# Kernel optimization log

Hardware: AMD Instinct MI355X
Metric: run time of the kernel (lower is better)

The kernel has to match this reference:

```python
import jax, jax.numpy as jnp
import numpy as np

B, C, H, W = 2, 24, 256, 256
R = 7  # window_size


def setup_inputs() -> dict:
    key = jax.random.key(0)
    k1, k2 = jax.random.split(key)
    latent = jax.random.normal(k1, (B, C, H, W), dtype=jnp.float32)
    # per-pixel, per-channel dynamic filter weights, one per window position (r*r)
    weights = jax.random.uniform(k2, (B, C, R * R, H, W), dtype=jnp.float32)
    return {"latent": latent, "weights": weights, "window_size": R}


def reference(latent, weights, window_size):
    """Faithful jax version of BaseTextureDiffusion._diffusion_step.

    torch: replicate-pad -> F.unfold (kernel r) -> view(B,C,r*r,H,W)
           -> permute -> elementwise * weights -> sum over r*r.
    F.unfold enumerates kernel offsets row-major (i*r + j), matching k below.
    Instead of materializing the r*r-times-larger windows tensor, accumulate
    the weighted shifted slices directly (same math, fused traffic).
    """
    r = window_size
    pad = r // 2
    h, w = latent.shape[2], latent.shape[3]
    padded = jnp.pad(latent, ((0, 0), (0, 0), (pad, pad), (pad, pad)), mode="edge")
    out = jnp.zeros_like(latent)
    for k in range(r * r):  # fixed small loop over kernel offsets
        i, j = divmod(k, r)
        out = out + weights[:, :, k] * padded[:, :, i:i + h, j:j + w]
    return out
```

## Files before the change

kernel.cpp:

```cpp
#include <hip/hip_runtime.h>


typedef float fx4 __attribute__((ext_vector_type(4)));

constexpr int Hh = 256, Ww = 256, Rr = 7, PAD = 3;
constexpr int TILE_H = 4;
constexpr int LW  = Ww + 2 * PAD;
constexpr int LWP = 264;
constexpr int LH  = TILE_H + 2 * PAD;
constexpr int TILES_Y = Hh / TILE_H;
constexpr int PLANES  = 48;

__global__ __launch_bounds__(256) void diffusion_kernel(
    const float* __restrict__ latent,
    const float* __restrict__ weights,
    float* __restrict__ out)
{
    __shared__ __align__(16) float lds[LH * LWP];

    const int bid   = blockIdx.x;
    const int plane = bid / TILES_Y;
    const int ty0   = (bid % TILES_Y) * TILE_H;

    const float* lat  = latent  + (size_t)plane * Hh * Ww;
    const float* wgt  = weights + (size_t)plane * (Rr * Rr) * Hh * Ww;
    float*       optr = out     + (size_t)plane * Hh * Ww;

    for (int idx = threadIdx.x; idx < LH * LW; idx += 256) {
        const int ly = idx / LW;
        const int lx = idx - ly * LW;
        const int gy = min(max(ty0 + ly - PAD, 0), Hh - 1);
        const int gx = min(max(lx - PAD, 0), Ww - 1);
        lds[ly * LWP + lx] = lat[gy * Ww + gx];
    }
    __syncthreads();

    const int tx = threadIdx.x & 63;
    const int ty = threadIdx.x >> 6;
    const int x  = 4 * tx;
    const int y  = ty0 + ty;

    const float* wbase = wgt + (size_t)y * Ww + x;

    fx4 acc = {0.f, 0.f, 0.f, 0.f};

    #pragma unroll
    for (int i = 0; i < Rr; ++i) {
        const float* lrow = &lds[(ty + i) * LWP + x];
        const float4 a = *(const float4*)(lrow);
        const float4 b = *(const float4*)(lrow + 4);
        const float2 c = *(const float2*)(lrow + 8);
        const float r[10] = {a.x, a.y, a.z, a.w, b.x, b.y, b.z, b.w, c.x, c.y};

        #pragma unroll
        for (int j = 0; j < Rr; ++j) {
            const int k = i * Rr + j;
            const fx4 w4 = __builtin_nontemporal_load(
                (const fx4*)(wbase + (size_t)k * (Hh * Ww)));
            acc.x += w4.x * r[j + 0];
            acc.y += w4.y * r[j + 1];
            acc.z += w4.z * r[j + 2];
            acc.w += w4.w * r[j + 3];
        }
    }

    __builtin_nontemporal_store(acc, (fx4*)(optr + (size_t)y * Ww + x));
}

extern "C" void kernel_launch(void* const* d_in, const int* in_sizes, int n_in,
                              void* d_out, int out_size, void* d_ws, size_t ws_size,
                              hipStream_t stream) {
    const float* latent  = (const float*)d_in[0];
    const float* weights = (const float*)d_in[1];
    float* out = (float*)d_out;

    const int nblocks = PLANES * TILES_Y;
    diffusion_kernel<<<nblocks, 256, 0, stream>>>(latent, weights, out);
}
```

Baseline: 757.5 us.

## Compute two output rows per thread and vectorize halo tile loading

Doubles the tile height so each thread accumulates two vertically adjacent output rows, letting one LDS row read feed both rows' filters and halving the halo overhead per block. The LDS fill now uses float4 global loads plus a small edge-replication pass, replacing scalar clamped loads. Weight loads switch from nontemporal to ordinary loads and are issued in groups of seven per row. The kernel stays bound by streaming the weights, and the extra registers and half as many blocks could reduce latency hiding.

```diff
diff --git a/kernel.cpp b/kernel.cpp
--- a/kernel.cpp
+++ b/kernel.cpp
@@ -4,10 +4,10 @@
 typedef float fx4 __attribute__((ext_vector_type(4)));
 
 constexpr int Hh = 256, Ww = 256, Rr = 7, PAD = 3;
-constexpr int TILE_H = 4;
-constexpr int LW  = Ww + 2 * PAD;
-constexpr int LWP = 264;
-constexpr int LH  = TILE_H + 2 * PAD;
+constexpr int TILE_H  = 8;
+constexpr int LH      = TILE_H + 2 * PAD;
+constexpr int LWP     = 272;
+constexpr int COL0    = 4;
 constexpr int TILES_Y = Hh / TILE_H;
 constexpr int PLANES  = 48;
 
@@ -26,45 +26,75 @@
     const float* wgt  = weights + (size_t)plane * (Rr * Rr) * Hh * Ww;
     float*       optr = out     + (size_t)plane * Hh * Ww;
 
-    for (int idx = threadIdx.x; idx < LH * LW; idx += 256) {
-        const int ly = idx / LW;
-        const int lx = idx - ly * LW;
+    for (int idx = threadIdx.x; idx < LH * 64; idx += 256) {
+        const int ly = idx >> 6;
+        const int q  = idx & 63;
         const int gy = min(max(ty0 + ly - PAD, 0), Hh - 1);
-        const int gx = min(max(lx - PAD, 0), Ww - 1);
-        lds[ly * LWP + lx] = lat[gy * Ww + gx];
+        const fx4 v  = *(const fx4*)(lat + (size_t)gy * Ww + 4 * q);
+        *(fx4*)(&lds[ly * LWP + COL0 + 4 * q]) = v;
+    }
+    if (threadIdx.x < LH * 6) {
+        const int ly  = threadIdx.x / 6;
+        const int h   = threadIdx.x % 6;
+        const int gy  = min(max(ty0 + ly - PAD, 0), Hh - 1);
+        const int col = (h < 3) ? (1 + h) : (257 + h);
+        const int gx  = (h < 3) ? 0 : (Ww - 1);
+        lds[ly * LWP + col] = lat[(size_t)gy * Ww + gx];
     }
     __syncthreads();
 
     const int tx = threadIdx.x & 63;
-    const int ty = threadIdx.x >> 6;
+    const int wy = threadIdx.x >> 6;
     const int x  = 4 * tx;
-    const int y  = ty0 + ty;
+    const int r0 = ty0 + 2 * wy;
 
-    const float* wbase = wgt + (size_t)y * Ww + x;
+    const float* w0 = wgt + (size_t)r0 * Ww + x;
+    const float* w1 = w0 + Ww;
 
-    fx4 acc = {0.f, 0.f, 0.f, 0.f};
+    fx4 acc0 = {0.f, 0.f, 0.f, 0.f};
+    fx4 acc1 = {0.f, 0.f, 0.f, 0.f};
 
     #pragma unroll
-    for (int i = 0; i < Rr; ++i) {
-        const float* lrow = &lds[(ty + i) * LWP + x];
-        const float4 a = *(const float4*)(lrow);
-        const float4 b = *(const float4*)(lrow + 4);
-        const float2 c = *(const float2*)(lrow + 8);
-        const float r[10] = {a.x, a.y, a.z, a.w, b.x, b.y, b.z, b.w, c.x, c.y};
+    for (int ii = 0; ii < 8; ++ii) {
+        const float* lrow = &lds[(2 * wy + ii) * LWP + x];
+        const fx4 a = *(const fx4*)(lrow);
+        const fx4 b = *(const fx4*)(lrow + 4);
+        const fx4 c = *(const fx4*)(lrow + 8);
+        const float l[12] = {a.x, a.y, a.z, a.w, b.x, b.y, b.z, b.w, c.x, c.y, c.z, c.w};
 
-        #pragma unroll
-        for (int j = 0; j < Rr; ++j) {
-            const int k = i * Rr + j;
-            const fx4 w4 = __builtin_nontemporal_load(
-                (const fx4*)(wbase + (size_t)k * (Hh * Ww)));
-            acc.x += w4.x * r[j + 0];
-            acc.y += w4.y * r[j + 1];
-            acc.z += w4.z * r[j + 2];
-            acc.w += w4.w * r[j + 3];
+        fx4 wa[7], wb[7];
+        if (ii < 7) {
+            #pragma unroll
+            for (int j = 0; j < 7; ++j)
+                wa[j] = *(const fx4*)(w0 + (size_t)(ii * 7 + j) * (Hh * Ww));
+        }
+        if (ii >= 1) {
+            #pragma unroll
+            for (int j = 0; j < 7; ++j)
+                wb[j] = *(const fx4*)(w1 + (size_t)((ii - 1) * 7 + j) * (Hh * Ww));
+        }
+        if (ii < 7) {
+            #pragma unroll
+            for (int j = 0; j < 7; ++j) {
+                acc0.x += wa[j].x * l[j + 1];
+                acc0.y += wa[j].y * l[j + 2];
+                acc0.z += wa[j].z * l[j + 3];
+                acc0.w += wa[j].w * l[j + 4];
+            }
+        }
+        if (ii >= 1) {
+            #pragma unroll
+            for (int j = 0; j < 7; ++j) {
+                acc1.x += wb[j].x * l[j + 1];
+                acc1.y += wb[j].y * l[j + 2];
+                acc1.z += wb[j].z * l[j + 3];
+                acc1.w += wb[j].w * l[j + 4];
+            }
         }
     }
 
-    __builtin_nontemporal_store(acc, (fx4*)(optr + (size_t)y * Ww + x));
+    __builtin_nontemporal_store(acc0, (fx4*)(optr + (size_t)r0 * Ww + x));
+    __builtin_nontemporal_store(acc1, (fx4*)(optr + (size_t)(r0 + 1) * Ww + x));
 }
 
 extern "C" void kernel_launch(void* const* d_in, const int* in_sizes, int n_in,
```

Result: slower. 778.7 us (+2.8%).
